# Optimization experiments

Hardware: AMD Instinct MI355X
Metric: run time of the kernel (lower is better)

The kernel has to match this reference:

```python
import jax, jax.numpy as jnp
import numpy as np

B, N, EB, NA, DIM, NIT = 256, 128, 5, 64, 512, 3  # EB = n_bonds + 1 (channel 0 = no-bond, dropped)


def setup_inputs() -> dict:
    key = jax.random.key(0)
    ks = jax.random.split(key, 10)
    adj = jax.random.uniform(ks[0], (B, N, N, EB), dtype=jnp.float32)
    node = jax.random.normal(ks[1], (B, N, NA), dtype=jnp.float32)
    hidden = jnp.zeros((B, N, DIM), dtype=jnp.float32)  # accepted but unused by forward
    # nn.Linear default init: U(-1/sqrt(fan_in), 1/sqrt(fan_in))
    se = 1.0 / np.sqrt(NA)
    sd = 1.0 / np.sqrt(DIM)
    W_embed = jax.random.uniform(ks[2], (NA, DIM), minval=-se, maxval=se, dtype=jnp.float32)
    b_embed = jax.random.uniform(ks[3], (DIM,), minval=-se, maxval=se, dtype=jnp.float32)
    W_layers = jax.random.uniform(ks[4], (NIT, DIM, DIM), minval=-sd, maxval=sd, dtype=jnp.float32)
    b_layers = jax.random.uniform(ks[5], (NIT, DIM), minval=-sd, maxval=sd, dtype=jnp.float32)
    W_out = jax.random.uniform(ks[6], (DIM, 1), minval=-sd, maxval=sd, dtype=jnp.float32)
    b_out = jax.random.uniform(ks[7], (1,), minval=-sd, maxval=sd, dtype=jnp.float32)
    return {"adj": adj, "hidden": hidden, "node": node,
            "W_embed": W_embed, "b_embed": b_embed,
            "W_layers": W_layers, "b_layers": b_layers,
            "W_out": W_out, "b_out": b_out}


def reference(adj, hidden, node, W_embed, b_embed, W_layers, b_layers, W_out, b_out):
    # adj[:, :, :, 1:].permute(0, 3, 1, 2) -> [B, E, N, N]
    a = jnp.transpose(adj[..., 1:], (0, 3, 1, 2))
    h = node @ W_embed + b_embed  # [B, N, DIM]
    for i in range(NIT):  # WLSLinearLayer: relu(Linear(h + sum_e adj_e @ h))
        agg = jnp.einsum('benm,bmd->bnd', a, h)  # sum over bond types of neighbor aggregation
        h = jax.nn.relu((h + agg) @ W_layers[i] + b_layers[i])
    graph_repr = jnp.mean(h, axis=1)  # [B, DIM]
    logit = graph_repr @ W_out + b_out  # [B, 1], activation=None path
    return (logit, graph_repr)
```

## Files before the change

### kernel.cpp

```cpp
#include <hip/hip_runtime.h>
#include <hip/hip_bf16.h>


typedef __bf16 bf16;
typedef __bf16 bf16x4 __attribute__((ext_vector_type(4)));
typedef __bf16 bf16x8 __attribute__((ext_vector_type(8)));
typedef float floatx4 __attribute__((ext_vector_type(4)));

__global__ __launch_bounds__(256) void k_asum(const float* __restrict__ adj,
                                              bf16* __restrict__ ahat) {
    int i = blockIdx.x * 256 + threadIdx.x;
    int base = i * 4;
    const float4* p = (const float4*)(adj + (size_t)base * 5);
    float4 v0 = p[0], v1 = p[1], v2 = p[2], v3 = p[3], v4 = p[4];
    float s[4];
    s[0] = v0.y + v0.z + v0.w + v1.x;
    s[1] = v1.z + v1.w + v2.x + v2.y;
    s[2] = v2.w + v3.x + v3.y + v3.z;
    s[3] = v4.x + v4.y + v4.z + v4.w;
    bf16x4 o;
#pragma unroll
    for (int j = 0; j < 4; j++) {
        int e = base + j;
        int m = e & 127, n = (e >> 7) & 127;
        float v = s[j] + ((n == m) ? 1.0f : 0.0f);
        o[j] = (bf16)v;
    }
    *(bf16x4*)(ahat + base) = o;
}

template <typename Tin>
__global__ __launch_bounds__(256) void k_transpose(const Tin* __restrict__ in, bf16* __restrict__ out,
                                                   int R, int C, long long sIn, long long sOut) {
    __shared__ bf16 tile[32][33];
    const Tin* src = in + (size_t)blockIdx.z * sIn;
    bf16* dst = out + (size_t)blockIdx.z * sOut;
    int c0 = blockIdx.x * 32, r0 = blockIdx.y * 32;
    int tx = threadIdx.x & 31, ty = threadIdx.x >> 5;
#pragma unroll
    for (int i = 0; i < 4; i++) {
        int r = ty + i * 8;
        tile[r][tx] = (bf16)(float)src[(size_t)(r0 + r) * C + c0 + tx];
    }
    __syncthreads();
#pragma unroll
    for (int i = 0; i < 4; i++) {
        int c = ty + i * 8;
        dst[(size_t)(c0 + c) * R + r0 + tx] = tile[tx][c];
    }
}

#define HTS 136
#define TBS 40

__global__ __launch_bounds__(1024, 4) void k_mega(
    const float* __restrict__ nodef,
    const bf16* __restrict__ Web_t,
    const float* __restrict__ b_embed,
    const bf16* __restrict__ Ahat,
    const bf16* __restrict__ Wlb_t,
    const float* __restrict__ b_layers,
    const float* __restrict__ W_out,
    const float* __restrict__ b_out,
    float* __restrict__ out)
{
    __shared__ __align__(16) bf16 HT[512 * HTS];
    __shared__ __align__(16) bf16 TB[128 * TBS];
    __shared__ float RsF[512];
    __shared__ float lpF[512];

    const int b = blockIdx.x;
    const int tid = threadIdx.x;
    const int lane = tid & 63, wid = tid >> 6;
    const int q = lane >> 4, l16 = lane & 15;

    const int dt = wid >> 3, ntw = wid & 7;
    bf16x8 ahf[4];
#pragma unroll
    for (int kk = 0; kk < 4; kk++)
        ahf[kk] = *(const bf16x8*)(Ahat + (size_t)b * 16384 +
                                   (size_t)(ntw * 16 + l16) * 128 + kk * 32 + q * 8);

    {
        const int wmE = wid >> 3, wnE = wid & 7;
        const float* Ab = nodef + (size_t)b * 8192;
        floatx4 accE[4][4] = {};
#pragma unroll
        for (int kk = 0; kk < 2; kk++) {
            bf16x8 af[4], bfr[4];
#pragma unroll
            for (int mt = 0; mt < 4; mt++) {
                const float* src = Ab + (size_t)(wmE * 64 + mt * 16 + l16) * 64 + kk * 32 + q * 8;
                float4 x = *(const float4*)src;
                float4 y = *(const float4*)(src + 4);
                bf16x8 v;
                v[0] = (bf16)x.x; v[1] = (bf16)x.y; v[2] = (bf16)x.z; v[3] = (bf16)x.w;
                v[4] = (bf16)y.x; v[5] = (bf16)y.y; v[6] = (bf16)y.z; v[7] = (bf16)y.w;
                af[mt] = v;
            }
#pragma unroll
            for (int nt = 0; nt < 4; nt++)
                bfr[nt] = *(const bf16x8*)(Web_t + (size_t)(wnE * 64 + nt * 16 + l16) * 64 + kk * 32 + q * 8);
#pragma unroll
            for (int mt = 0; mt < 4; mt++)
#pragma unroll
                for (int nt = 0; nt < 4; nt++)
                    accE[mt][nt] = __builtin_amdgcn_mfma_f32_16x16x32_bf16(af[mt], bfr[nt], accE[mt][nt], 0, 0, 0);
        }
#pragma unroll
        for (int mt = 0; mt < 4; mt++)
#pragma unroll
            for (int nt = 0; nt < 4; nt++) {
                int d = wnE * 64 + nt * 16 + l16;
                float bv = b_embed[d];
                int n0 = wmE * 64 + mt * 16 + q * 4;
                bf16x4 pk;
#pragma unroll
                for (int r = 0; r < 4; r++) pk[r] = (bf16)(accE[mt][nt][r] + bv);
                *(bf16x4*)&HT[d * HTS + n0] = pk;
            }
    }
    __syncthreads();

    for (int it = 0; it < 3; it++) {
        const bf16* WT = Wlb_t + (size_t)it * 262144;
        const float* bl = b_layers + it * 512;
        floatx4 acc[8][2] = {};

        for (int dc = 0; dc < 16; dc++) {
            floatx4 a1 = {};
            {
                int drow = dc * 32 + dt * 16 + l16;
#pragma unroll
                for (int kk = 0; kk < 4; kk++) {
                    bf16x8 af = *(const bf16x8*)&HT[drow * HTS + kk * 32 + q * 8];
                    a1 = __builtin_amdgcn_mfma_f32_16x16x32_bf16(af, ahf[kk], a1, 0, 0, 0);
                }
            }
            bf16x8 bfr[2];
#pragma unroll
            for (int nt = 0; nt < 2; nt++)
                bfr[nt] = *(const bf16x8*)(WT + (size_t)(wid * 32 + nt * 16 + l16) * 512 + dc * 32 + q * 8);
            {
                bf16x4 pk;
#pragma unroll
                for (int r = 0; r < 4; r++) pk[r] = (bf16)a1[r];
                *(bf16x4*)&TB[(ntw * 16 + l16) * TBS + dt * 16 + q * 4] = pk;
            }
            __syncthreads();

#pragma unroll
            for (int mt = 0; mt < 8; mt++) {
                bf16x8 af2 = *(const bf16x8*)&TB[(mt * 16 + l16) * TBS + q * 8];
#pragma unroll
                for (int nt = 0; nt < 2; nt++)
                    acc[mt][nt] = __builtin_amdgcn_mfma_f32_16x16x32_bf16(af2, bfr[nt], acc[mt][nt], 0, 0, 0);
            }
            __syncthreads();
        }

        if (it < 2) {
#pragma unroll
            for (int nt = 0; nt < 2; nt++) {
                int dp = wid * 32 + nt * 16 + l16;
                float bv = bl[dp];
#pragma unroll
                for (int mt = 0; mt < 8; mt++) {
                    int n0 = mt * 16 + q * 4;
                    bf16x4 pk;
#pragma unroll
                    for (int r = 0; r < 4; r++) pk[r] = (bf16)fmaxf(acc[mt][nt][r] + bv, 0.f);
                    *(bf16x4*)&HT[dp * HTS + n0] = pk;
                }
            }
            __syncthreads();
        } else {
#pragma unroll
            for (int nt = 0; nt < 2; nt++) {
                int dp = wid * 32 + nt * 16 + l16;
                float bv = bl[dp];
                float s = 0.f;
#pragma unroll
                for (int mt = 0; mt < 8; mt++)
#pragma unroll
                    for (int r = 0; r < 4; r++)
                        s += fmaxf(acc[mt][nt][r] + bv, 0.f);
                s += __shfl_down(s, 32);
                s += __shfl_down(s, 16);
                if (lane < 16) RsF[wid * 32 + nt * 16 + lane] = s;
            }
        }
    }
    __syncthreads();

    if (tid < 512) {
        float g = RsF[tid] * (1.f / 128.f);
        out[256 + (size_t)b * 512 + tid] = g;
        lpF[tid] = g * W_out[tid];
    }
    __syncthreads();
    for (int s = 256; s > 0; s >>= 1) {
        if (tid < s) lpF[tid] += lpF[tid + s];
        __syncthreads();
    }
    if (tid == 0) out[b] = lpF[0] + b_out[0];
}

extern "C" void kernel_launch(void* const* d_in, const int* in_sizes, int n_in,
                              void* d_out, int out_size, void* d_ws, size_t ws_size,
                              hipStream_t stream) {
    const float* adj      = (const float*)d_in[0];
    const float* node     = (const float*)d_in[2];
    const float* W_embed  = (const float*)d_in[3];
    const float* b_embed  = (const float*)d_in[4];
    const float* W_layers = (const float*)d_in[5];
    const float* b_layers = (const float*)d_in[6];
    const float* W_out    = (const float*)d_in[7];
    const float* b_out    = (const float*)d_in[8];
    float* out = (float*)d_out;

    char* ws = (char*)d_ws;
    bf16* Web_t = (bf16*)(ws);
    bf16* Wlb_t = (bf16*)(ws + 65536);
    bf16* Ahat  = (bf16*)(ws + 1638400);

    k_transpose<float><<<dim3(16, 2, 1), 256, 0, stream>>>(W_embed, Web_t, 64, 512, 0, 0);
    k_transpose<float><<<dim3(16, 16, 3), 256, 0, stream>>>(W_layers, Wlb_t, 512, 512, 262144, 262144);
    k_asum<<<4096, 256, 0, stream>>>(adj, Ahat);
    k_mega<<<256, 1024, 0, stream>>>(node, Web_t, b_embed, Ahat, Wlb_t, b_layers,
                                     W_out, b_out, out);
}
```

Baseline: 270.4 us.

## Fuse adjacency sum into mega kernel, swizzle HT layout, retile layer GEMM

The adjacency bond-channel reduction is now computed inside the main per-graph kernel and staged in shared memory, so the separate k_asum pass and its global bf16 round-trip go away. The two weight-transpose launches are merged into one kernel. The H^T shared buffer drops its padding in favour of an XOR swizzle, which lets all LDS buffers share one pool. The layer GEMM is retiled so each wave computes 64x64 instead of 128x32, giving more MFMA reuse per loaded fragment but needing a two-way partial sum for the final mean. The trade-off is that each block now reads its 320KB adjacency slice at kernel start without overlap, plus extra syncs.

New measurement: 328.1 us. 1.21x slower.

```diff
diff --git a/kernel.cpp b/kernel.cpp
--- a/kernel.cpp
+++ b/kernel.cpp
@@ -7,40 +7,27 @@
 typedef __bf16 bf16x8 __attribute__((ext_vector_type(8)));
 typedef float floatx4 __attribute__((ext_vector_type(4)));
 
-__global__ __launch_bounds__(256) void k_asum(const float* __restrict__ adj,
-                                              bf16* __restrict__ ahat) {
-    int i = blockIdx.x * 256 + threadIdx.x;
-    int base = i * 4;
-    const float4* p = (const float4*)(adj + (size_t)base * 5);
-    float4 v0 = p[0], v1 = p[1], v2 = p[2], v3 = p[3], v4 = p[4];
-    float s[4];
-    s[0] = v0.y + v0.z + v0.w + v1.x;
-    s[1] = v1.z + v1.w + v2.x + v2.y;
-    s[2] = v2.w + v3.x + v3.y + v3.z;
-    s[3] = v4.x + v4.y + v4.z + v4.w;
-    bf16x4 o;
-#pragma unroll
-    for (int j = 0; j < 4; j++) {
-        int e = base + j;
-        int m = e & 127, n = (e >> 7) & 127;
-        float v = s[j] + ((n == m) ? 1.0f : 0.0f);
-        o[j] = (bf16)v;
-    }
-    *(bf16x4*)(ahat + base) = o;
-}
-
-template <typename Tin>
-__global__ __launch_bounds__(256) void k_transpose(const Tin* __restrict__ in, bf16* __restrict__ out,
-                                                   int R, int C, long long sIn, long long sOut) {
+#define TBS 40
+#define AS  136
+
+__global__ __launch_bounds__(256) void k_wt(const float* __restrict__ We,
+                                            const float* __restrict__ Wl,
+                                            bf16* __restrict__ WeT,
+                                            bf16* __restrict__ WlT) {
     __shared__ bf16 tile[32][33];
-    const Tin* src = in + (size_t)blockIdx.z * sIn;
-    bf16* dst = out + (size_t)blockIdx.z * sOut;
+    int z = blockIdx.z;
+    const float* src;
+    bf16* dst;
+    int R;
+    if (z < 3) { src = Wl + (size_t)z * 262144; dst = WlT + (size_t)z * 262144; R = 512; }
+    else       { src = We;                      dst = WeT;                      R = 64; }
     int c0 = blockIdx.x * 32, r0 = blockIdx.y * 32;
+    if (r0 >= R) return;
     int tx = threadIdx.x & 31, ty = threadIdx.x >> 5;
 #pragma unroll
     for (int i = 0; i < 4; i++) {
         int r = ty + i * 8;
-        tile[r][tx] = (bf16)(float)src[(size_t)(r0 + r) * C + c0 + tx];
+        tile[r][tx] = (bf16)src[(size_t)(r0 + r) * 512 + c0 + tx];
     }
     __syncthreads();
 #pragma unroll
@@ -50,36 +37,55 @@
     }
 }
 
-#define HTS 136
-#define TBS 40
-
 __global__ __launch_bounds__(1024, 4) void k_mega(
+    const float* __restrict__ adj,
     const float* __restrict__ nodef,
     const bf16* __restrict__ Web_t,
     const float* __restrict__ b_embed,
-    const bf16* __restrict__ Ahat,
     const bf16* __restrict__ Wlb_t,
     const float* __restrict__ b_layers,
     const float* __restrict__ W_out,
     const float* __restrict__ b_out,
     float* __restrict__ out)
 {
-    __shared__ __align__(16) bf16 HT[512 * HTS];
-    __shared__ __align__(16) bf16 TB[128 * TBS];
-    __shared__ float RsF[512];
-    __shared__ float lpF[512];
+    __shared__ __align__(16) char pool[141312];
+    bf16* HT = (bf16*)pool;
+    bf16* TB = (bf16*)(pool + 131072);
 
     const int b = blockIdx.x;
     const int tid = threadIdx.x;
     const int lane = tid & 63, wid = tid >> 6;
     const int q = lane >> 4, l16 = lane & 15;
 
+    bf16* AhatL = (bf16*)pool;
+    {
+        const float4* srcb = (const float4*)(adj + (size_t)b * 81920);
+#pragma unroll
+        for (int p = 0; p < 4; p++) {
+            int t = p * 1024 + tid;
+            const float4* ptr = srcb + (size_t)t * 5;
+            float4 v0 = ptr[0], v1 = ptr[1], v2 = ptr[2], v3 = ptr[3], v4 = ptr[4];
+            float s0 = v0.y + v0.z + v0.w + v1.x;
+            float s1 = v1.z + v1.w + v2.x + v2.y;
+            float s2 = v2.w + v3.x + v3.y + v3.z;
+            float s3 = v4.x + v4.y + v4.z + v4.w;
+            int n = t >> 5, m0 = (t & 31) * 4;
+            bf16x4 o;
+            o[0] = (bf16)(s0 + ((n == m0 + 0) ? 1.f : 0.f));
+            o[1] = (bf16)(s1 + ((n == m0 + 1) ? 1.f : 0.f));
+            o[2] = (bf16)(s2 + ((n == m0 + 2) ? 1.f : 0.f));
+            o[3] = (bf16)(s3 + ((n == m0 + 3) ? 1.f : 0.f));
+            *(bf16x4*)&AhatL[n * AS + m0] = o;
+        }
+    }
+    __syncthreads();
+
     const int dt = wid >> 3, ntw = wid & 7;
     bf16x8 ahf[4];
 #pragma unroll
     for (int kk = 0; kk < 4; kk++)
-        ahf[kk] = *(const bf16x8*)(Ahat + (size_t)b * 16384 +
-                                   (size_t)(ntw * 16 + l16) * 128 + kk * 32 + q * 8);
+        ahf[kk] = *(const bf16x8*)&AhatL[(ntw * 16 + l16) * AS + kk * 32 + q * 8];
+    __syncthreads();
 
     {
         const int wmE = wid >> 3, wnE = wid & 7;
@@ -90,9 +96,9 @@
             bf16x8 af[4], bfr[4];
 #pragma unroll
             for (int mt = 0; mt < 4; mt++) {
-                const float* src = Ab + (size_t)(wmE * 64 + mt * 16 + l16) * 64 + kk * 32 + q * 8;
-                float4 x = *(const float4*)src;
-                float4 y = *(const float4*)(src + 4);
+                const float* srcp = Ab + (size_t)(wmE * 64 + mt * 16 + l16) * 64 + kk * 32 + q * 8;
+                float4 x = *(const float4*)srcp;
+                float4 y = *(const float4*)(srcp + 4);
                 bf16x8 v;
                 v[0] = (bf16)x.x; v[1] = (bf16)x.y; v[2] = (bf16)x.z; v[3] = (bf16)x.w;
                 v[4] = (bf16)y.x; v[5] = (bf16)y.y; v[6] = (bf16)y.z; v[7] = (bf16)y.w;
@@ -113,34 +119,39 @@
             for (int nt = 0; nt < 4; nt++) {
                 int d = wnE * 64 + nt * 16 + l16;
                 float bv = b_embed[d];
-                int n0 = wmE * 64 + mt * 16 + q * 4;
+                int c = wmE * 8 + mt * 2 + (q >> 1);
+                int off = ((c ^ (d & 15)) << 3) + (q & 1) * 4;
                 bf16x4 pk;
 #pragma unroll
                 for (int r = 0; r < 4; r++) pk[r] = (bf16)(accE[mt][nt][r] + bv);
-                *(bf16x4*)&HT[d * HTS + n0] = pk;
-            }
-    }
-    __syncthreads();
+                *(bf16x4*)&HT[d * 128 + off] = pk;
+            }
+    }
+    __syncthreads();
+
+    const int nw = wid & 1, dw = wid >> 1;
 
     for (int it = 0; it < 3; it++) {
         const bf16* WT = Wlb_t + (size_t)it * 262144;
         const float* bl = b_layers + it * 512;
-        floatx4 acc[8][2] = {};
+        floatx4 acc[4][4] = {};
 
         for (int dc = 0; dc < 16; dc++) {
+            bf16x8 bfr[4];
+#pragma unroll
+            for (int nt = 0; nt < 4; nt++)
+                bfr[nt] = *(const bf16x8*)(WT + (size_t)(dw * 64 + nt * 16 + l16) * 512 + dc * 32 + q * 8);
+
             floatx4 a1 = {};
             {
                 int drow = dc * 32 + dt * 16 + l16;
 #pragma unroll
                 for (int kk = 0; kk < 4; kk++) {
-                    bf16x8 af = *(const bf16x8*)&HT[drow * HTS + kk * 32 + q * 8];
+                    int off = ((4 * kk + q) ^ (drow & 15)) << 3;
+                    bf16x8 af = *(const bf16x8*)&HT[drow * 128 + off];
                     a1 = __builtin_amdgcn_mfma_f32_16x16x32_bf16(af, ahf[kk], a1, 0, 0, 0);
                 }
             }
-            bf16x8 bfr[2];
-#pragma unroll
-            for (int nt = 0; nt < 2; nt++)
-                bfr[nt] = *(const bf16x8*)(WT + (size_t)(wid * 32 + nt * 16 + l16) * 512 + dc * 32 + q * 8);
             {
                 bf16x4 pk;
 #pragma unroll
@@ -149,52 +160,58 @@
             }
             __syncthreads();
 
-#pragma unroll
-            for (int mt = 0; mt < 8; mt++) {
-                bf16x8 af2 = *(const bf16x8*)&TB[(mt * 16 + l16) * TBS + q * 8];
-#pragma unroll
-                for (int nt = 0; nt < 2; nt++)
-                    acc[mt][nt] = __builtin_amdgcn_mfma_f32_16x16x32_bf16(af2, bfr[nt], acc[mt][nt], 0, 0, 0);
-            }
+            bf16x8 af2[4];
+#pragma unroll
+            for (int mt = 0; mt < 4; mt++)
+                af2[mt] = *(const bf16x8*)&TB[(nw * 64 + mt * 16 + l16) * TBS + q * 8];
+#pragma unroll
+            for (int nt = 0; nt < 4; nt++)
+#pragma unroll
+                for (int mt = 0; mt < 4; mt++)
+                    acc[mt][nt] = __builtin_amdgcn_mfma_f32_16x16x32_bf16(af2[mt], bfr[nt], acc[mt][nt], 0, 0, 0);
             __syncthreads();
         }
 
         if (it < 2) {
 #pragma unroll
-            for (int nt = 0; nt < 2; nt++) {
-                int dp = wid * 32 + nt * 16 + l16;
+            for (int nt = 0; nt < 4; nt++) {
+                int dp = dw * 64 + nt * 16 + l16;
                 float bv = bl[dp];
 #pragma unroll
-                for (int mt = 0; mt < 8; mt++) {
-                    int n0 = mt * 16 + q * 4;
+                for (int mt = 0; mt < 4; mt++) {
+                    int c = nw * 8 + mt * 2 + (q >> 1);
+                    int off = ((c ^ (dp & 15)) << 3) + (q & 1) * 4;
                     bf16x4 pk;
 #pragma unroll
                     for (int r = 0; r < 4; r++) pk[r] = (bf16)fmaxf(acc[mt][nt][r] + bv, 0.f);
-                    *(bf16x4*)&HT[dp * HTS + n0] = pk;
+                    *(bf16x4*)&HT[dp * 128 + off] = pk;
                 }
             }
             __syncthreads();
         } else {
-#pragma unroll
-            for (int nt = 0; nt < 2; nt++) {
-                int dp = wid * 32 + nt * 16 + l16;
+            float* RsF = (float*)(pool + 131072);
+#pragma unroll
+            for (int nt = 0; nt < 4; nt++) {
+                int dp = dw * 64 + nt * 16 + l16;
                 float bv = bl[dp];
                 float s = 0.f;
 #pragma unroll
-                for (int mt = 0; mt < 8; mt++)
+                for (int mt = 0; mt < 4; mt++)
 #pragma unroll
                     for (int r = 0; r < 4; r++)
                         s += fmaxf(acc[mt][nt][r] + bv, 0.f);
                 s += __shfl_down(s, 32);
                 s += __shfl_down(s, 16);
-                if (lane < 16) RsF[wid * 32 + nt * 16 + lane] = s;
-            }
-        }
-    }
-    __syncthreads();
-
+                if (lane < 16) RsF[nw * 512 + dp] = s;
+            }
+        }
+    }
+    __syncthreads();
+
+    float* RsF = (float*)(pool + 131072);
+    float* lpF = (float*)(pool + 131072 + 4096);
     if (tid < 512) {
-        float g = RsF[tid] * (1.f / 128.f);
+        float g = (RsF[tid] + RsF[512 + tid]) * (1.f / 128.f);
         out[256 + (size_t)b * 512 + tid] = g;
         lpF[tid] = g * W_out[tid];
     }
@@ -222,11 +239,8 @@
     char* ws = (char*)d_ws;
     bf16* Web_t = (bf16*)(ws);
     bf16* Wlb_t = (bf16*)(ws + 65536);
-    bf16* Ahat  = (bf16*)(ws + 1638400);
-
-    k_transpose<float><<<dim3(16, 2, 1), 256, 0, stream>>>(W_embed, Web_t, 64, 512, 0, 0);
-    k_transpose<float><<<dim3(16, 16, 3), 256, 0, stream>>>(W_layers, Wlb_t, 512, 512, 262144, 262144);
-    k_asum<<<4096, 256, 0, stream>>>(adj, Ahat);
-    k_mega<<<256, 1024, 0, stream>>>(node, Web_t, b_embed, Ahat, Wlb_t, b_layers,
+
+    k_wt<<<dim3(16, 16, 4), 256, 0, stream>>>(W_embed, W_layers, Web_t, Wlb_t);
+    k_mega<<<256, 1024, 0, stream>>>(adj, node, Web_t, b_embed, Wlb_t, b_layers,
                                      W_out, b_out, out);
 }
```
